# Optimization experiments

Measured on AMD Instinct MI355X. Metric: run time of the kernel, lower is better.

The kernel has to match this reference:

```python
import jax, jax.numpy as jnp
from jax import lax
import numpy as np

IMG = 500
FM = 31
RATIOS = [1.0, 2.0, 0.5]
SCALES = [128, 256, 512]
PRE_NMS = 6000
POST_NMS = 1500  # train_nms_topn (test=False)
IOU_THR = 0.7
VARIANCES = np.array([0.1, 0.1, 0.2, 0.2], np.float32)
BATCH = 16


def _gen_anchors():
    # bbox_utils.generate_anchors: normalized [y1,x1,y2,x2], grid of 31x31 centers,
    # 9 base shapes from (scale, ratio), clipped to [0,1].
    ctr = (np.arange(FM, dtype=np.float32) + 0.5) / FM
    cy, cx = np.meshgrid(ctr, ctr, indexing='ij')          # [FM,FM]
    base = []
    for s in SCALES:
        for r in RATIOS:
            w = s * np.sqrt(r) / IMG
            h = s / np.sqrt(r) / IMG
            base.append([h, w])
    base = np.array(base, np.float32)                       # [9,2]
    h, w = base[:, 0], base[:, 1]
    cy = cy[..., None]; cx = cx[..., None]                  # [FM,FM,1]
    anc = np.stack([cy - h / 2, cx - w / 2, cy + h / 2, cx + w / 2], axis=-1)
    return np.clip(anc.reshape(-1, 4), 0.0, 1.0).astype(np.float32)  # [8649,4]


def setup_inputs() -> dict:
    key = jax.random.key(0)
    k1, k2 = jax.random.split(key)
    return {
        'rpn_bbox_deltas': jax.random.normal(k1, (BATCH, FM, FM, 36), jnp.float32),
        'rpn_probs': jax.random.uniform(k2, (BATCH, FM, FM, 9), jnp.float32),
        'anchors': jnp.asarray(_gen_anchors()),
    }


def _nms_keep(boxes, scores):
    # Greedy NMS over score-descending-sorted boxes; returns keep mask [N].
    N = boxes.shape[0]
    y1, x1, y2, x2 = boxes[:, 0], boxes[:, 1], boxes[:, 2], boxes[:, 3]
    area = (y2 - y1) * (x2 - x1)

    def body(i, state):
        supp, keep, cnt = state
        valid = jnp.logical_and(jnp.logical_not(supp[i]), cnt < POST_NMS)
        keep = keep.at[i].set(valid)
        cnt = cnt + valid.astype(jnp.int32)
        ih = jnp.maximum(jnp.minimum(y2[i], y2) - jnp.maximum(y1[i], y1), 0.0)
        iw = jnp.maximum(jnp.minimum(x2[i], x2) - jnp.maximum(x1[i], x1), 0.0)
        inter = ih * iw
        iou = inter / (area[i] + area - inter + 1e-8)
        supp = jnp.where(valid, jnp.logical_or(supp, iou > IOU_THR), supp)
        return supp, keep, cnt

    supp0 = jnp.zeros((N,), bool)
    keep0 = jnp.zeros((N,), bool)
    _, keep, _ = lax.fori_loop(0, N, body, (supp0, keep0, jnp.int32(0)))
    return keep


def reference(rpn_bbox_deltas, rpn_probs, anchors):
    B = rpn_bbox_deltas.shape[0]
    N = anchors.shape[0]
    deltas = rpn_bbox_deltas.reshape(B, N, 4) * jnp.asarray(VARIANCES)  # [B,N,4]
    probs = rpn_probs.reshape(B, N)                                     # [B,N]

    # decode anchor deltas -> boxes
    anc_h = anchors[:, 2] - anchors[:, 0]
    anc_w = anchors[:, 3] - anchors[:, 1]
    ctr_y = anchors[:, 0] + 0.5 * anc_h
    ctr_x = anchors[:, 1] + 0.5 * anc_w
    bh = jnp.exp(deltas[..., 2]) * anc_h
    bw = jnp.exp(deltas[..., 3]) * anc_w
    bcy = deltas[..., 0] * anc_h + ctr_y
    bcx = deltas[..., 1] * anc_w + ctr_x
    y1 = bcy - 0.5 * bh
    x1 = bcx - 0.5 * bw
    boxes = jnp.stack([y1, x1, y1 + bh, x1 + bw], axis=-1)              # [B,N,4]

    # pre-NMS top-k by objectness (sorted descending)
    top_scores, top_idx = lax.top_k(probs, PRE_NMS)                     # [B,PRE_NMS]
    top_boxes = jnp.take_along_axis(boxes, top_idx[..., None], axis=1)  # [B,PRE_NMS,4]

    # greedy NMS (selection is non-differentiable, compute on stopped values)
    keep = jax.vmap(_nms_keep)(lax.stop_gradient(top_boxes),
                               lax.stop_gradient(top_scores))           # [B,PRE_NMS] bool

    # compact kept entries to the front, zero-pad to POST_NMS (combined NMS semantics)
    rank = jnp.cumsum(keep, axis=1) - 1
    slot = jnp.where(keep, rank, POST_NMS)  # dropped entries go to overflow slot

    def _scatter(sl, bx, sc, k):
        ob = jnp.zeros((POST_NMS + 1, 4), bx.dtype).at[sl].set(jnp.where(k[:, None], bx, 0.0))
        os = jnp.zeros((POST_NMS + 1,), sc.dtype).at[sl].set(jnp.where(k, sc, 0.0))
        return ob[:POST_NMS], os[:POST_NMS]

    roi_bboxes, roi_scores = jax.vmap(_scatter)(slot, top_boxes, top_scores, keep)
    roi_bboxes = jnp.clip(roi_bboxes, 0.0, 1.0)  # clip_boxes=True in combined NMS
    return roi_bboxes, roi_scores
```

## Files before the change

kernel.cpp:

```cpp
#include <hip/hip_runtime.h>
#include <hip/hip_bf16.h>

#define BATCH   16
#define N_ANC   8649
#define SORT_N  16384
#define PRE     6000
#define POST    1500
#define ROWW    188
#define MROWS   6016
#define NGRP    188
#define GLIM    64
#define TI      256
#define TJ      256

__global__ __launch_bounds__(256) void k_decode(
    const float* __restrict__ deltas, const float* __restrict__ probs,
    const float* __restrict__ anchors, float4* __restrict__ boxes,
    unsigned long long* __restrict__ keys)
{
    int t = blockIdx.x * 256 + threadIdx.x;
    if (t >= BATCH * SORT_N) return;
    int b = t / SORT_N;
    int n = t - b * SORT_N;
    if (n >= N_ANC) { keys[t] = ~0ULL; return; }

    float s = probs[(size_t)b * N_ANC + n];
    unsigned int bits = __float_as_uint(s);
    unsigned int u = bits ^ ((bits & 0x80000000u) ? 0xFFFFFFFFu : 0x80000000u);
    keys[(size_t)b * SORT_N + n] = ((unsigned long long)(~u) << 32) | (unsigned int)n;

    float4 a = ((const float4*)anchors)[n];
    float4 d = ((const float4*)deltas)[(size_t)b * N_ANC + n];
    float dy = d.x * 0.1f, dx = d.y * 0.1f, dh = d.z * 0.2f, dw = d.w * 0.2f;
    float ah = a.z - a.x, aw = a.w - a.y;
    float cy = a.x + 0.5f * ah, cx = a.y + 0.5f * aw;
    float bh = expf(dh) * ah, bw = expf(dw) * aw;
    float bcy = dy * ah + cy, bcx = dx * aw + cx;
    float y1 = bcy - 0.5f * bh, x1 = bcx - 0.5f * bw;
    boxes[(size_t)b * N_ANC + n] = make_float4(y1, x1, y1 + bh, x1 + bw);
}

__global__ __launch_bounds__(1024) void k_sort(unsigned long long* __restrict__ keys)
{
    __shared__ unsigned long long sb[8192];
    int b = blockIdx.x;
    unsigned long long* kb = keys + (size_t)b * SORT_N;

    for (int c = 0; c < 2; c++) {
        unsigned long long* g = kb + c * 8192;
        for (int t = threadIdx.x; t < 8192; t += 1024) sb[t] = g[t];
        __syncthreads();
        for (int k = 2; k <= 8192; k <<= 1) {
            for (int j = k >> 1; j >= 1; j >>= 1) {
                for (int p = threadIdx.x; p < 4096; p += 1024) {
                    int i  = ((p & ~(j - 1)) << 1) | (p & (j - 1));
                    int gi = (c << 13) | i;
                    bool asc = ((gi & k) == 0);
                    unsigned long long a = sb[i], b2 = sb[i | j];
                    bool sw = asc ? (a > b2) : (a < b2);
                    if (sw) { sb[i] = b2; sb[i | j] = a; }
                }
                __syncthreads();
            }
        }
        for (int t = threadIdx.x; t < 8192; t += 1024) g[t] = sb[t];
        __syncthreads();
    }

    for (int p = threadIdx.x; p < 8192; p += 1024) {
        unsigned long long a = kb[p], b2 = kb[p + 8192];
        if (a > b2) { kb[p] = b2; kb[p + 8192] = a; }
    }
    __syncthreads();

    for (int t = threadIdx.x; t < 8192; t += 1024) sb[t] = kb[t];
    __syncthreads();
    for (int j = 4096; j >= 1; j >>= 1) {
        for (int p = threadIdx.x; p < 4096; p += 1024) {
            int i = ((p & ~(j - 1)) << 1) | (p & (j - 1));
            unsigned long long a = sb[i], b2 = sb[i | j];
            if (a > b2) { sb[i] = b2; sb[i | j] = a; }
        }
        __syncthreads();
    }
    for (int t = threadIdx.x; t < 6016; t += 1024) kb[t] = sb[t];
}

__global__ __launch_bounds__(256) void k_gather(
    const unsigned long long* __restrict__ keys, const float4* __restrict__ boxes,
    const float* __restrict__ probs,
    float4* __restrict__ sboxes, float* __restrict__ sscores)
{
    int t = blockIdx.x * 256 + threadIdx.x;
    if (t >= BATCH * PRE) return;
    int b = t / PRE;
    int r = t - b * PRE;
    unsigned long long k = keys[(size_t)b * SORT_N + r];
    int idx = (int)(k & 0xFFFFFFFFu);
    sboxes[(size_t)b * PRE + r]  = boxes[(size_t)b * N_ANC + idx];
    sscores[(size_t)b * PRE + r] = probs[(size_t)b * N_ANC + idx];
}

template<int IT0, bool CHK>
__global__ __launch_bounds__(256) void k_iou(
    const float4* __restrict__ sboxes, unsigned int* __restrict__ mask,
    unsigned int* __restrict__ diag, const int* __restrict__ done)
{
    int it = IT0 + blockIdx.x;
    int jt = blockIdx.y;
    int b  = blockIdx.z;
    if (jt < it) return;
    if (CHK && done[b]) return;

    __shared__ float4 jb[TJ];
    __shared__ float  ja[TJ];
    int t = threadIdx.x;
    int j = jt * TJ + t;
    float4 bj = (j < PRE) ? sboxes[(size_t)b * PRE + j]
                          : make_float4(-2e6f, -2e6f, -1.5e6f, -1.5e6f);
    jb[t] = bj;
    ja[t] = (bj.z - bj.x) * (bj.w - bj.y);
    __syncthreads();

    int i = it * TI + t;
    if (i >= PRE) return;
    float4 bi = sboxes[(size_t)b * PRE + i];
    float areai = (bi.z - bi.x) * (bi.w - bi.y);

    unsigned int w[8];
    if (jt > it) {
        for (int wq = 0; wq < 8; wq++) {
            unsigned int bits = 0u;
            #pragma unroll
            for (int jj = 0; jj < 32; jj++) {
                int lj = wq * 32 + jj;
                float4 bx = jb[lj];
                float ih = fmaxf(fminf(bi.z, bx.z) - fmaxf(bi.x, bx.x), 0.0f);
                float iw = fmaxf(fminf(bi.w, bx.w) - fmaxf(bi.y, bx.y), 0.0f);
                float inter = ih * iw;
                float iou = inter / (areai + ja[lj] - inter + 1e-8f);
                if (iou > 0.7f) bits |= (1u << jj);
            }
            w[wq] = bits;
        }
    } else {
        unsigned int dw = 0u;
        for (int wq = 0; wq < 8; wq++) {
            int jbase = jt * TJ + wq * 32;
            unsigned int bits = 0u;
            if (jbase + 31 > i) {
                #pragma unroll
                for (int jj = 0; jj < 32; jj++) {
                    int lj = wq * 32 + jj;
                    float4 bx = jb[lj];
                    float ih = fmaxf(fminf(bi.z, bx.z) - fmaxf(bi.x, bx.x), 0.0f);
                    float iw = fmaxf(fminf(bi.w, bx.w) - fmaxf(bi.y, bx.y), 0.0f);
                    float inter = ih * iw;
                    float iou = inter / (areai + ja[lj] - inter + 1e-8f);
                    if (iou > 0.7f && (jbase + jj) > i) bits |= (1u << jj);
                }
            }
            w[wq] = bits;
            if (wq == (t >> 5)) dw = bits;
        }
        diag[(size_t)b * MROWS + it * 256 + t] = dw;
    }

    unsigned int* row = mask + ((size_t)b * MROWS + i) * ROWW + jt * 8;
    ((uint4*)row)[0] = make_uint4(w[0], w[1], w[2], w[3]);
    if (jt < 23) ((uint4*)row)[1] = make_uint4(w[4], w[5], w[6], w[7]);
}

__global__ __launch_bounds__(64, 1) void k_scan_a(
    const unsigned int* __restrict__ mask, const unsigned int* __restrict__ diag,
    int* __restrict__ out_idx, int* __restrict__ out_cnt,
    uint4* __restrict__ stbuf, int* __restrict__ done)
{
    int b = blockIdx.x;
    int lane = threadIdx.x;
    const unsigned int* mb = mask + (size_t)b * MROWS * ROWW;
    const unsigned int* db = diag + (size_t)b * MROWS;
    bool lact = (lane < 47);
    unsigned int lbit  = 1u << (lane & 31);
    unsigned int below = lbit - 1u;

    uint4 st = make_uint4(0, 0, 0, 0);
    int cnt = 0;
    int* oi = out_idx + b * POST;

    for (int g = 0; g < GLIM; g++) {
        const uint4* dt = (const uint4*)(db + g * 32);
        uint4 t0 = dt[0], t1 = dt[1], t2 = dt[2], t3 = dt[3];
        uint4 t4 = dt[4], t5 = dt[5], t6 = dt[6], t7 = dt[7];

        bool need = lact && (4 * lane + 3 >= g);
        const unsigned int* gp = mb + (size_t)g * 32 * ROWW + 4 * lane;
        uint4 r[32];
        #pragma unroll
        for (int k = 0; k < 32; k++)
            r[k] = need ? *(const uint4*)(gp + (size_t)k * ROWW)
                        : make_uint4(0, 0, 0, 0);

        unsigned int cword = (g & 2) ? ((g & 1) ? st.w : st.z)
                                     : ((g & 1) ? st.y : st.x);
        unsigned int swv = __shfl(cword, g >> 2);

        unsigned int tri[32];
        tri[0]=t0.x;  tri[1]=t0.y;  tri[2]=t0.z;  tri[3]=t0.w;
        tri[4]=t1.x;  tri[5]=t1.y;  tri[6]=t1.z;  tri[7]=t1.w;
        tri[8]=t2.x;  tri[9]=t2.y;  tri[10]=t2.z; tri[11]=t2.w;
        tri[12]=t3.x; tri[13]=t3.y; tri[14]=t3.z; tri[15]=t3.w;
        tri[16]=t4.x; tri[17]=t4.y; tri[18]=t4.z; tri[19]=t4.w;
        tri[20]=t5.x; tri[21]=t5.y; tri[22]=t5.z; tri[23]=t5.w;
        tri[24]=t6.x; tri[25]=t6.y; tri[26]=t6.z; tri[27]=t6.w;
        tri[28]=t7.x; tri[29]=t7.y; tri[30]=t7.z; tri[31]=t7.w;

        unsigned int alive = ~swv;
        unsigned int keepm = 0;
        #pragma unroll
        for (int k = 0; k < 32; k++) {
            unsigned int bit = (alive >> k) & 1u;
            keepm |= bit << k;
            alive &= ~((0u - bit) & tri[k]);
        }

        int need_n = POST - cnt;
        int rank = __popc(keepm & below);
        bool keep_me = (lane < 32) && (keepm & lbit) && (rank < need_n);
        unsigned long long bal = __ballot(keep_me);
        unsigned int keepm2 = (unsigned int)bal;
        if (keep_me) oi[cnt + rank] = g * 32 + lane;

        #pragma unroll
        for (int k = 0; k < 32; k++) {
            unsigned int m = 0u - ((keepm2 >> k) & 1u);
            st.x |= r[k].x & m; st.y |= r[k].y & m;
            st.z |= r[k].z & m; st.w |= r[k].w & m;
        }
        cnt += __popc(keepm2);
    }

    if (lact) stbuf[b * 47 + lane] = st;
    if (lane == 0) { out_cnt[b] = cnt; done[b] = (cnt >= POST) ? 1 : 0; }
}

__global__ __launch_bounds__(64, 1) void k_scan_b(
    const unsigned int* __restrict__ mask, const unsigned int* __restrict__ diag,
    int* __restrict__ out_idx, int* __restrict__ out_cnt,
    const uint4* __restrict__ stbuf, const int* __restrict__ done)
{
    int b = blockIdx.x;
    if (done[b]) return;
    int lane = threadIdx.x;
    const unsigned int* mb = mask + (size_t)b * MROWS * ROWW;
    const unsigned int* db = diag + (size_t)b * MROWS;
    bool lact = (lane < 47);
    unsigned int lbit  = 1u << (lane & 31);
    unsigned int below = lbit - 1u;

    uint4 st = lact ? stbuf[b * 47 + lane] : make_uint4(0, 0, 0, 0);
    int cnt = out_cnt[b];
    int* oi = out_idx + b * POST;

    for (int g = GLIM; g < NGRP; g++) {
        const uint4* dt = (const uint4*)(db + g * 32);
        uint4 t0 = dt[0], t1 = dt[1], t2 = dt[2], t3 = dt[3];
        uint4 t4 = dt[4], t5 = dt[5], t6 = dt[6], t7 = dt[7];

        bool need = lact && (4 * lane + 3 >= g);
        const unsigned int* gp = mb + (size_t)g * 32 * ROWW + 4 * lane;
        uint4 r[32];
        #pragma unroll
        for (int k = 0; k < 32; k++)
            r[k] = need ? *(const uint4*)(gp + (size_t)k * ROWW)
                        : make_uint4(0, 0, 0, 0);

        unsigned int cword = (g & 2) ? ((g & 1) ? st.w : st.z)
                                     : ((g & 1) ? st.y : st.x);
        unsigned int swv = __shfl(cword, g >> 2);

        unsigned int tri[32];
        tri[0]=t0.x;  tri[1]=t0.y;  tri[2]=t0.z;  tri[3]=t0.w;
        tri[4]=t1.x;  tri[5]=t1.y;  tri[6]=t1.z;  tri[7]=t1.w;
        tri[8]=t2.x;  tri[9]=t2.y;  tri[10]=t2.z; tri[11]=t2.w;
        tri[12]=t3.x; tri[13]=t3.y; tri[14]=t3.z; tri[15]=t3.w;
        tri[16]=t4.x; tri[17]=t4.y; tri[18]=t4.z; tri[19]=t4.w;
        tri[20]=t5.x; tri[21]=t5.y; tri[22]=t5.z; tri[23]=t5.w;
        tri[24]=t6.x; tri[25]=t6.y; tri[26]=t6.z; tri[27]=t6.w;
        tri[28]=t7.x; tri[29]=t7.y; tri[30]=t7.z; tri[31]=t7.w;

        unsigned int valid = (g == NGRP - 1) ? 0xFFFFu : 0xFFFFFFFFu;
        unsigned int alive = ~swv & valid;
        unsigned int keepm = 0;
        #pragma unroll
        for (int k = 0; k < 32; k++) {
            unsigned int bit = (alive >> k) & 1u;
            keepm |= bit << k;
            alive &= ~((0u - bit) & tri[k]);
        }

        int need_n = POST - cnt;
        int rank = __popc(keepm & below);
        bool keep_me = (lane < 32) && (keepm & lbit) && (rank < need_n);
        unsigned long long bal = __ballot(keep_me);
        unsigned int keepm2 = (unsigned int)bal;
        if (keep_me) oi[cnt + rank] = g * 32 + lane;

        #pragma unroll
        for (int k = 0; k < 32; k++) {
            unsigned int m = 0u - ((keepm2 >> k) & 1u);
            st.x |= r[k].x & m; st.y |= r[k].y & m;
            st.z |= r[k].z & m; st.w |= r[k].w & m;
        }
        cnt += __popc(keepm2);
        if (cnt >= POST) break;
    }
    if (lane == 0) out_cnt[b] = cnt;
}

__global__ __launch_bounds__(256) void k_out(
    const float4* __restrict__ sboxes, const float* __restrict__ sscores,
    const int* __restrict__ out_idx, const int* __restrict__ out_cnt,
    float* __restrict__ out)
{
    int t = blockIdx.x * 256 + threadIdx.x;
    if (t >= BATCH * POST) return;
    int b = t / POST;
    int r = t - b * POST;
    float4 v = make_float4(0, 0, 0, 0);
    float sc = 0.f;
    if (r < out_cnt[b]) {
        int i = out_idx[b * POST + r];
        float4 bx = sboxes[(size_t)b * PRE + i];
        v.x = fminf(fmaxf(bx.x, 0.f), 1.f);
        v.y = fminf(fmaxf(bx.y, 0.f), 1.f);
        v.z = fminf(fmaxf(bx.z, 0.f), 1.f);
        v.w = fminf(fmaxf(bx.w, 0.f), 1.f);
        sc = sscores[(size_t)b * PRE + i];
    }
    ((float4*)out)[t] = v;
    out[(size_t)BATCH * POST * 4 + t] = sc;
}

extern "C" void kernel_launch(void* const* d_in, const int* in_sizes, int n_in,
                              void* d_out, int out_size, void* d_ws, size_t ws_size,
                              hipStream_t stream)
{
    const float* deltas  = (const float*)d_in[0];
    const float* probs   = (const float*)d_in[1];
    const float* anchors = (const float*)d_in[2];
    float* out = (float*)d_out;

    char* ws = (char*)d_ws;
    size_t off = 0;
    auto alloc = [&](size_t bytes) {
        size_t o = off;
        off = (off + bytes + 255) & ~(size_t)255;
        return o;
    };
    float4* boxes            = (float4*)(ws + alloc((size_t)BATCH * N_ANC * 16));
    unsigned long long* keys = (unsigned long long*)(ws + alloc((size_t)BATCH * SORT_N * 8));
    float4* sboxes           = (float4*)(ws + alloc((size_t)BATCH * PRE * 16));
    float* sscores           = (float*)(ws + alloc((size_t)BATCH * PRE * 4));
    unsigned int* mask       = (unsigned int*)(ws + alloc((size_t)BATCH * MROWS * ROWW * 4));
    unsigned int* diag       = (unsigned int*)(ws + alloc((size_t)BATCH * MROWS * 4));
    int* oidx                = (int*)(ws + alloc((size_t)BATCH * POST * 4));
    int* ocnt                = (int*)(ws + alloc((size_t)BATCH * 4));
    uint4* stbuf             = (uint4*)(ws + alloc((size_t)BATCH * 47 * 16));
    int* done                = (int*)(ws + alloc((size_t)BATCH * 4));

    k_decode<<<(BATCH * SORT_N + 255) / 256, 256, 0, stream>>>(deltas, probs, anchors, boxes, keys);
    k_sort<<<BATCH, 1024, 0, stream>>>(keys);
    k_gather<<<(BATCH * PRE + 255) / 256, 256, 0, stream>>>(keys, boxes, probs, sboxes, sscores);
    k_iou<0, false><<<dim3(8, 24, BATCH), 256, 0, stream>>>(sboxes, mask, diag, done);
    k_scan_a<<<BATCH, 64, 0, stream>>>(mask, diag, oidx, ocnt, stbuf, done);
    k_iou<8, true><<<dim3(16, 24, BATCH), 256, 0, stream>>>(sboxes, mask, diag, done);
    k_scan_b<<<BATCH, 64, 0, stream>>>(mask, diag, oidx, ocnt, stbuf, done);
    k_out<<<(BATCH * POST + 255) / 256, 256, 0, stream>>>(sboxes, sscores, oidx, ocnt, out);
}
```

Baseline: 779.2 us.

## Split bitonic sort across blocks and shrink first-phase IoU to leading tile square

The per-batch sort now runs its two 8192-key chunk sorts in separate blocks, which doubles sort parallelism, and a separate kernel does the final merge. The first IoU pass now computes only the top-left 8x8 tile square, so the first scan can start sooner and reads only the first 16 lanes of mask columns. The second IoU pass fills in all remaining tiles, and only for batches that still need more boxes. The second scan rebuilds its suppression state by OR-ing the mask rows of already-kept boxes instead of loading a saved state buffer, which adds a serial loop of up to cnt row loads.

```diff
diff --git a/kernel.cpp b/kernel.cpp
--- a/kernel.cpp
+++ b/kernel.cpp
@@ -40,32 +40,36 @@
     boxes[(size_t)b * N_ANC + n] = make_float4(y1, x1, y1 + bh, x1 + bw);
 }
 
-__global__ __launch_bounds__(1024) void k_sort(unsigned long long* __restrict__ keys)
+__global__ __launch_bounds__(1024) void k_sort_chunk(unsigned long long* __restrict__ keys)
+{
+    __shared__ unsigned long long sb[8192];
+    int b = blockIdx.x >> 1;
+    int c = blockIdx.x & 1;
+    unsigned long long* g = keys + (size_t)b * SORT_N + c * 8192;
+
+    for (int t = threadIdx.x; t < 8192; t += 1024) sb[t] = g[t];
+    __syncthreads();
+    for (int k = 2; k <= 8192; k <<= 1) {
+        for (int j = k >> 1; j >= 1; j >>= 1) {
+            for (int p = threadIdx.x; p < 4096; p += 1024) {
+                int i  = ((p & ~(j - 1)) << 1) | (p & (j - 1));
+                int gi = (c << 13) | i;
+                bool asc = ((gi & k) == 0);
+                unsigned long long a = sb[i], b2 = sb[i | j];
+                bool sw = asc ? (a > b2) : (a < b2);
+                if (sw) { sb[i] = b2; sb[i | j] = a; }
+            }
+            __syncthreads();
+        }
+    }
+    for (int t = threadIdx.x; t < 8192; t += 1024) g[t] = sb[t];
+}
+
+__global__ __launch_bounds__(1024) void k_sort_merge(unsigned long long* __restrict__ keys)
 {
     __shared__ unsigned long long sb[8192];
     int b = blockIdx.x;
     unsigned long long* kb = keys + (size_t)b * SORT_N;
-
-    for (int c = 0; c < 2; c++) {
-        unsigned long long* g = kb + c * 8192;
-        for (int t = threadIdx.x; t < 8192; t += 1024) sb[t] = g[t];
-        __syncthreads();
-        for (int k = 2; k <= 8192; k <<= 1) {
-            for (int j = k >> 1; j >= 1; j >>= 1) {
-                for (int p = threadIdx.x; p < 4096; p += 1024) {
-                    int i  = ((p & ~(j - 1)) << 1) | (p & (j - 1));
-                    int gi = (c << 13) | i;
-                    bool asc = ((gi & k) == 0);
-                    unsigned long long a = sb[i], b2 = sb[i | j];
-                    bool sw = asc ? (a > b2) : (a < b2);
-                    if (sw) { sb[i] = b2; sb[i | j] = a; }
-                }
-                __syncthreads();
-            }
-        }
-        for (int t = threadIdx.x; t < 8192; t += 1024) g[t] = sb[t];
-        __syncthreads();
-    }
 
     for (int p = threadIdx.x; p < 8192; p += 1024) {
         unsigned long long a = kb[p], b2 = kb[p + 8192];
@@ -101,16 +105,19 @@
     sscores[(size_t)b * PRE + r] = probs[(size_t)b * N_ANC + idx];
 }
 
-template<int IT0, bool CHK>
+template<bool FIRST>
 __global__ __launch_bounds__(256) void k_iou(
     const float4* __restrict__ sboxes, unsigned int* __restrict__ mask,
     unsigned int* __restrict__ diag, const int* __restrict__ done)
 {
-    int it = IT0 + blockIdx.x;
+    int it = blockIdx.x;
     int jt = blockIdx.y;
     int b  = blockIdx.z;
     if (jt < it) return;
-    if (CHK && done[b]) return;
+    if (!FIRST) {
+        if (it < 8 && jt < 8) return;
+        if (done[b]) return;
+    }
 
     __shared__ float4 jb[TJ];
     __shared__ float  ja[TJ];
@@ -173,14 +180,12 @@
 
 __global__ __launch_bounds__(64, 1) void k_scan_a(
     const unsigned int* __restrict__ mask, const unsigned int* __restrict__ diag,
-    int* __restrict__ out_idx, int* __restrict__ out_cnt,
-    uint4* __restrict__ stbuf, int* __restrict__ done)
+    int* __restrict__ out_idx, int* __restrict__ out_cnt, int* __restrict__ done)
 {
     int b = blockIdx.x;
     int lane = threadIdx.x;
     const unsigned int* mb = mask + (size_t)b * MROWS * ROWW;
     const unsigned int* db = diag + (size_t)b * MROWS;
-    bool lact = (lane < 47);
     unsigned int lbit  = 1u << (lane & 31);
     unsigned int below = lbit - 1u;
 
@@ -193,7 +198,7 @@
         uint4 t0 = dt[0], t1 = dt[1], t2 = dt[2], t3 = dt[3];
         uint4 t4 = dt[4], t5 = dt[5], t6 = dt[6], t7 = dt[7];
 
-        bool need = lact && (4 * lane + 3 >= g);
+        bool need = (lane < 16) && (4 * lane + 3 >= g);
         const unsigned int* gp = mb + (size_t)g * 32 * ROWW + 4 * lane;
         uint4 r[32];
         #pragma unroll
@@ -240,14 +245,12 @@
         cnt += __popc(keepm2);
     }
 
-    if (lact) stbuf[b * 47 + lane] = st;
     if (lane == 0) { out_cnt[b] = cnt; done[b] = (cnt >= POST) ? 1 : 0; }
 }
 
 __global__ __launch_bounds__(64, 1) void k_scan_b(
     const unsigned int* __restrict__ mask, const unsigned int* __restrict__ diag,
-    int* __restrict__ out_idx, int* __restrict__ out_cnt,
-    const uint4* __restrict__ stbuf, const int* __restrict__ done)
+    int* __restrict__ out_idx, int* __restrict__ out_cnt, const int* __restrict__ done)
 {
     int b = blockIdx.x;
     if (done[b]) return;
@@ -258,9 +261,18 @@
     unsigned int lbit  = 1u << (lane & 31);
     unsigned int below = lbit - 1u;
 
-    uint4 st = lact ? stbuf[b * 47 + lane] : make_uint4(0, 0, 0, 0);
     int cnt = out_cnt[b];
     int* oi = out_idx + b * POST;
+
+    uint4 st = make_uint4(0, 0, 0, 0);
+    bool hi = (lane >= 16) && lact;
+    for (int c = 0; c < cnt; c++) {
+        int idx = oi[c];
+        if (hi) {
+            uint4 v = *(const uint4*)(mb + (size_t)idx * ROWW + 4 * lane);
+            st.x |= v.x; st.y |= v.y; st.z |= v.z; st.w |= v.w;
+        }
+    }
 
     for (int g = GLIM; g < NGRP; g++) {
         const uint4* dt = (const uint4*)(db + g * 32);
@@ -366,15 +378,15 @@
     unsigned int* diag       = (unsigned int*)(ws + alloc((size_t)BATCH * MROWS * 4));
     int* oidx                = (int*)(ws + alloc((size_t)BATCH * POST * 4));
     int* ocnt                = (int*)(ws + alloc((size_t)BATCH * 4));
-    uint4* stbuf             = (uint4*)(ws + alloc((size_t)BATCH * 47 * 16));
     int* done                = (int*)(ws + alloc((size_t)BATCH * 4));
 
     k_decode<<<(BATCH * SORT_N + 255) / 256, 256, 0, stream>>>(deltas, probs, anchors, boxes, keys);
-    k_sort<<<BATCH, 1024, 0, stream>>>(keys);
+    k_sort_chunk<<<BATCH * 2, 1024, 0, stream>>>(keys);
+    k_sort_merge<<<BATCH, 1024, 0, stream>>>(keys);
     k_gather<<<(BATCH * PRE + 255) / 256, 256, 0, stream>>>(keys, boxes, probs, sboxes, sscores);
-    k_iou<0, false><<<dim3(8, 24, BATCH), 256, 0, stream>>>(sboxes, mask, diag, done);
-    k_scan_a<<<BATCH, 64, 0, stream>>>(mask, diag, oidx, ocnt, stbuf, done);
-    k_iou<8, true><<<dim3(16, 24, BATCH), 256, 0, stream>>>(sboxes, mask, diag, done);
-    k_scan_b<<<BATCH, 64, 0, stream>>>(mask, diag, oidx, ocnt, stbuf, done);
+    k_iou<true><<<dim3(8, 8, BATCH), 256, 0, stream>>>(sboxes, mask, diag, done);
+    k_scan_a<<<BATCH, 64, 0, stream>>>(mask, diag, oidx, ocnt, done);
+    k_iou<false><<<dim3(24, 24, BATCH), 256, 0, stream>>>(sboxes, mask, diag, done);
+    k_scan_b<<<BATCH, 64, 0, stream>>>(mask, diag, oidx, ocnt, done);
     k_out<<<(BATCH * POST + 255) / 256, 256, 0, stream>>>(sboxes, sscores, oidx, ocnt, out);
 }
```

Result: slower. 991.9 us (+27.3%).
